# Kernel optimization log

Measured on AMD Instinct MI355X. Metric: run time of the kernel, lower is better.

The kernel has to match this reference:

```python
import jax, jax.numpy as jnp
import numpy as np

B, L, H, E = 4, 2048, 8, 64

def setup_inputs() -> dict:
    key = jax.random.key(0)
    kq, kk, kv = jax.random.split(key, 3)
    queries = jax.random.normal(kq, (B, L, H, E), dtype=jnp.float32)
    keys = jax.random.normal(kk, (B, L, H, E), dtype=jnp.float32)
    values = jax.random.normal(kv, (B, L, H, E), dtype=jnp.float32)
    return {"queries": queries, "keys": keys, "values": values}

def reference(queries, keys, values):
    # queries/keys/values: [B, L, H, E]
    E_ = queries.shape[-1]
    scale = 1.0 / jnp.sqrt(jnp.float32(E_))
    # scores: [B, H, L, S]
    scores = jnp.einsum('blhe,bshe->bhls', queries, keys)
    Lq, S = scores.shape[-2], scores.shape[-1]
    # TriangularCausalMask: mask positions where s > l (strict upper triangle)
    causal = jnp.tril(jnp.ones((Lq, S), dtype=bool))
    scores = jnp.where(causal, scores, -jnp.inf)
    A = jax.nn.softmax(scale * scores, axis=-1)  # dropout p=0 -> identity
    V = jnp.einsum('bhls,bshd->blhd', A, values)
    return V
```

## Files before the change

### kernel.cpp

```cpp
#include <hip/hip_runtime.h>
#include <hip/hip_bf16.h>


#define Bc 4
#define Lc 2048
#define Hc 8
#define Ec 64
#define TB 64
#define NT (Lc / TB)
#define BH_BYTES (NT * TB * Ec * 2)
#define WS_V_OFF ((size_t)32 * BH_BYTES)

using f32x4 = __attribute__((ext_vector_type(4))) float;
using f16x8 = __attribute__((ext_vector_type(8))) _Float16;
using f16x4 = __attribute__((ext_vector_type(4))) _Float16;
using hf16x2 = __fp16 __attribute__((ext_vector_type(2)));

static __device__ __forceinline__ unsigned int pk2(float lo, float hi) {
    union { hf16x2 h; unsigned int u; } c;
    c.h = __builtin_amdgcn_cvt_pkrtz(lo, hi);
    return c.u;
}

static __device__ __forceinline__ void gload16(const void* g, void* l) {
    __builtin_amdgcn_global_load_lds(
        (const __attribute__((address_space(1))) unsigned int*)g,
        (__attribute__((address_space(3))) unsigned int*)l, 16, 0, 0);
}

__global__ __launch_bounds__(256)
void prep_kernel(const float* __restrict__ K, const float* __restrict__ V,
                 char* __restrict__ ws)
{
    __shared__ char vstage[64 * 144];

    const int bid = blockIdx.x;
    const int bh = bid >> 5, kt = bid & 31;
    const int b = bh >> 3, h = bh & 7;
    const int tid = threadIdx.x;
    const int r = tid >> 2, q4 = tid & 3;
    const int c0 = 16 * q4;
    const size_t base_bh = (size_t)b * Lc * Hc * Ec + (size_t)h * Ec;
    const int kbase = kt * TB;
    char* kimg = ws + (size_t)bh * BH_BYTES + (size_t)kt * 8192;
    char* vimg = ws + WS_V_OFF + (size_t)bh * BH_BYTES + (size_t)kt * 8192;

    const int rs = (r & 7) << 4;
    {
        const float* kp = K + base_bh + (size_t)(kbase + r) * 512 + c0;
        unsigned int w[8];
        #pragma unroll
        for (int i = 0; i < 4; ++i) {
            float4 f = *(const float4*)(kp + 4 * i);
            w[2*i]   = pk2(f.x, f.y);
            w[2*i+1] = pk2(f.z, f.w);
        }
        *(uint4*)(kimg + r * 128 + ((32*q4)      ^ rs)) = *(uint4*)&w[0];
        *(uint4*)(kimg + r * 128 + ((32*q4 + 16) ^ rs)) = *(uint4*)&w[4];
    }
    {
        const float* vp = V + base_bh + (size_t)(kbase + r) * 512 + c0;
        unsigned int w[8];
        #pragma unroll
        for (int i = 0; i < 4; ++i) {
            float4 f = *(const float4*)(vp + 4 * i);
            w[2*i]   = pk2(f.x, f.y);
            w[2*i+1] = pk2(f.z, f.w);
        }
        *(uint4*)(vstage + r * 144 + 32*q4)      = *(uint4*)&w[0];
        *(uint4*)(vstage + r * 144 + 32*q4 + 16) = *(uint4*)&w[4];
    }
    __syncthreads();
    {
        const int e = tid >> 2, kq = tid & 3, kv0 = 16 * kq;
        unsigned int w[8];
        #pragma unroll
        for (int i = 0; i < 8; ++i) {
            unsigned int lo = *(const unsigned short*)(vstage + (kv0 + 2*i)     * 144 + 2*e);
            unsigned int hi = *(const unsigned short*)(vstage + (kv0 + 2*i + 1) * 144 + 2*e);
            w[i] = lo | (hi << 16);
        }
        const int es = (e & 7) << 4;
        *(uint4*)(vimg + e * 128 + ((32*kq)      ^ es)) = *(uint4*)&w[0];
        *(uint4*)(vimg + e * 128 + ((32*kq + 16) ^ es)) = *(uint4*)&w[4];
    }
}

__global__ __launch_bounds__(128, 3)
void fa_fwd_kernel(const float* __restrict__ Q, const char* __restrict__ ws,
                   float* __restrict__ Out)
{
    __shared__ char klds[2 * 8192];
    __shared__ char vlds[2 * 8192];

    const int bid = blockIdx.x;
    const int qi  = bid >> 5;
    const int bh  = bid & 31;
    const int b   = bh >> 3, h = bh & 7;
    const int qt  = (NT - 1) - qi;
    const int qbase = qt * TB;

    const int tid  = threadIdx.x;
    const int wid  = tid >> 6;
    const int lane = tid & 63;
    const int l15  = lane & 15;
    const int l4   = lane >> 4;

    const size_t base_bh = (size_t)b * Lc * Hc * Ec + (size_t)h * Ec;
    const char* kimg = ws + (size_t)bh * BH_BYTES;
    const char* vimg = ws + WS_V_OFF + (size_t)bh * BH_BYTES;
    const float SL2E = 0.125f * 1.44269504088896340736f;

    const int sw  = (l15 & 7) << 4;
    const int ko0 = l15 * 128 + ((16 * l4)      ^ sw);
    const int ko1 = l15 * 128 + ((64 + 16 * l4) ^ sw);
    int vo[4];
    #pragma unroll
    for (int m = 0; m < 4; ++m) vo[m] = l15 * 128 + ((32 * m + 8 * l4) ^ sw);

    f16x4 ones;
    {
        const _Float16 ov = (_Float16)((l15 == 0) ? 1.0f : 0.0f);
        ones[0] = ov; ones[1] = ov; ones[2] = ov; ones[3] = ov;
    }

    const int stoff = tid * 16;

    f16x8 qa[2][2];
    #pragma unroll
    for (int g = 0; g < 2; ++g) {
        const int qrow = qbase + 32 * wid + 16 * g + l15;
        const float* qpr = Q + base_bh + (size_t)qrow * 512 + 8 * l4;
        float4 f0 = *(const float4*)(qpr);
        float4 f1 = *(const float4*)(qpr + 4);
        float4 f2 = *(const float4*)(qpr + 32);
        float4 f3 = *(const float4*)(qpr + 36);
        union { f16x8 v; unsigned int u[4]; } pk;
        pk.u[0] = pk2(f0.x * SL2E, f0.y * SL2E);
        pk.u[1] = pk2(f0.z * SL2E, f0.w * SL2E);
        pk.u[2] = pk2(f1.x * SL2E, f1.y * SL2E);
        pk.u[3] = pk2(f1.z * SL2E, f1.w * SL2E);
        qa[g][0] = pk.v;
        pk.u[0] = pk2(f2.x * SL2E, f2.y * SL2E);
        pk.u[1] = pk2(f2.z * SL2E, f2.w * SL2E);
        pk.u[2] = pk2(f3.x * SL2E, f3.y * SL2E);
        pk.u[3] = pk2(f3.z * SL2E, f3.w * SL2E);
        qa[g][1] = pk.v;
    }

    f32x4 o[2][4] = {};
    f32x4 ol[2] = {};
    float m_run[2] = {-1e30f, -1e30f};

    #pragma unroll
    for (int j = 0; j < 4; ++j) {
        gload16(kimg + stoff + j * 2048, klds + stoff + j * 2048);
        gload16(vimg + stoff + j * 2048, vlds + stoff + j * 2048);
    }
    __syncthreads();

    for (int kt = 0; kt <= qt; ++kt) {
        const int cur = kt & 1;
        const char* kb = klds + cur * 8192;
        const char* vb = vlds + cur * 8192;

        if (kt < qt) {
            const char* ks = kimg + (size_t)(kt + 1) * 8192;
            const char* vs = vimg + (size_t)(kt + 1) * 8192;
            char* kd = klds + (cur ^ 1) * 8192;
            char* vd = vlds + (cur ^ 1) * 8192;
            #pragma unroll
            for (int j = 0; j < 4; ++j) {
                gload16(ks + stoff + j * 2048, kd + stoff + j * 2048);
                gload16(vs + stoff + j * 2048, vd + stoff + j * 2048);
            }
        }

        f32x4 s[2][4];
        #pragma unroll
        for (int n = 0; n < 4; ++n) {
            f16x8 a0 = *(const f16x8*)(kb + n * 2048 + ko0);
            f16x8 a1 = *(const f16x8*)(kb + n * 2048 + ko1);
            #pragma unroll
            for (int g = 0; g < 2; ++g) {
                f32x4 z = {0.f, 0.f, 0.f, 0.f};
                z = __builtin_amdgcn_mfma_f32_16x16x32_f16(a0, qa[g][0], z, 0, 0, 0);
                z = __builtin_amdgcn_mfma_f32_16x16x32_f16(a1, qa[g][1], z, 0, 0, 0);
                s[g][n] = z;
            }
        }

        if (kt == qt) {
            #pragma unroll
            for (int g = 0; g < 2; ++g) {
                const int q_g = qbase + 32 * wid + 16 * g + l15;
                #pragma unroll
                for (int n = 0; n < 4; ++n) {
                    #pragma unroll
                    for (int r = 0; r < 4; ++r) {
                        const int kv_g = kt * TB + 16 * n + 4 * l4 + r;
                        if (kv_g > q_g) s[g][n][r] = -1e30f;
                    }
                }
            }
        }

        float pmax[2];
        #pragma unroll
        for (int g = 0; g < 2; ++g) {
            float a0 = fmaxf(s[g][0][0], s[g][0][1]), a1 = fmaxf(s[g][0][2], s[g][0][3]);
            float a2 = fmaxf(s[g][1][0], s[g][1][1]), a3 = fmaxf(s[g][1][2], s[g][1][3]);
            float a4 = fmaxf(s[g][2][0], s[g][2][1]), a5 = fmaxf(s[g][2][2], s[g][2][3]);
            float a6 = fmaxf(s[g][3][0], s[g][3][1]), a7 = fmaxf(s[g][3][2], s[g][3][3]);
            float pm = fmaxf(fmaxf(fmaxf(a0, a1), fmaxf(a2, a3)),
                             fmaxf(fmaxf(a4, a5), fmaxf(a6, a7)));
            pm = fmaxf(pm, __shfl_xor(pm, 16, 64));
            pm = fmaxf(pm, __shfl_xor(pm, 32, 64));
            pmax[g] = pm;
        }

        #pragma unroll
        for (int g = 0; g < 2; ++g) {
            if (!__all(pmax[g] - m_run[g] <= 8.0f)) {
                const float m_new = fmaxf(m_run[g], pmax[g]);
                const float fac = __builtin_exp2f(m_run[g] - m_new);
                m_run[g] = m_new;
                float fr[4];
                #pragma unroll
                for (int r = 0; r < 4; ++r) fr[r] = __shfl(fac, 4 * l4 + r, 64);
                #pragma unroll
                for (int c = 0; c < 4; ++c)
                    #pragma unroll
                    for (int r = 0; r < 4; ++r) o[g][c][r] *= fr[r];
                #pragma unroll
                for (int r = 0; r < 4; ++r) ol[g][r] *= fr[r];
            }
        }

        unsigned int ph[2][4][2];
        #pragma unroll
        for (int g = 0; g < 2; ++g) {
            #pragma unroll
            for (int n = 0; n < 4; ++n) {
                float p0 = __builtin_exp2f(s[g][n][0] - m_run[g]);
                float p1 = __builtin_exp2f(s[g][n][1] - m_run[g]);
                float p2 = __builtin_exp2f(s[g][n][2] - m_run[g]);
                float p3 = __builtin_exp2f(s[g][n][3] - m_run[g]);
                ph[g][n][0] = pk2(p0, p1);
                ph[g][n][1] = pk2(p2, p3);
            }
        }

        #pragma unroll
        for (int m = 0; m < 4; ++m) {
            f16x4 vbf[4];
            #pragma unroll
            for (int c = 0; c < 4; ++c)
                vbf[c] = *(const f16x4*)(vb + c * 2048 + vo[m]);
            #pragma unroll
            for (int g = 0; g < 2; ++g) {
                union { f16x4 h; unsigned int u[2]; } pa;
                pa.u[0] = ph[g][m][0]; pa.u[1] = ph[g][m][1];
                ol[g] = __builtin_amdgcn_mfma_f32_16x16x16f16(pa.h, ones, ol[g], 0, 0, 0);
                #pragma unroll
                for (int c = 0; c < 4; ++c)
                    o[g][c] = __builtin_amdgcn_mfma_f32_16x16x16f16(pa.h, vbf[c], o[g][c], 0, 0, 0);
            }
        }
        __syncthreads();
    }

    float* op = Out + base_bh;
    #pragma unroll
    for (int g = 0; g < 2; ++g) {
        float ir[4];
        #pragma unroll
        for (int r = 0; r < 4; ++r) {
            const float iv = 1.0f / ol[g][r];
            ir[r] = __shfl(iv, 16 * l4, 64);
        }
        const int qrow0 = qbase + 32 * wid + 16 * g;
        #pragma unroll
        for (int c = 0; c < 4; ++c)
            #pragma unroll
            for (int r = 0; r < 4; ++r)
                op[(size_t)(qrow0 + 4 * l4 + r) * 512 + 16 * c + l15] = o[g][c][r] * ir[r];
    }
}

extern "C" void kernel_launch(void* const* d_in, const int* in_sizes, int n_in,
                              void* d_out, int out_size, void* d_ws, size_t ws_size,
                              hipStream_t stream) {
    const float* Q = (const float*)d_in[0];
    const float* K = (const float*)d_in[1];
    const float* V = (const float*)d_in[2];
    float* O = (float*)d_out;
    char* ws = (char*)d_ws;
    hipLaunchKernelGGL(prep_kernel, dim3(Bc * Hc * NT), dim3(256), 0, stream, K, V, ws);
    hipLaunchKernelGGL(fa_fwd_kernel, dim3(NT * Bc * Hc), dim3(128), 0, stream, Q, ws, O);
}
```

Before: 73.30 us.

## Pre-swizzle K/V into MFMA fragment order and load straight to registers

The prep kernel now writes K and V tiles in the exact per-lane MFMA operand layout, so the attention kernel loads them directly from global memory into registers instead of staging them through LDS with barriers. The attention kernel becomes single-wave blocks of 32 query rows (2048 blocks), mapped so each XCD handles a contiguous set of batch-heads for L2 locality, and it prefetches the next K/V tile into registers. This removes LDS traffic and __syncthreads, but raises register pressure and depends on cache bandwidth to keep the per-wave global loads from stalling.

```diff
diff --git a/kernel.cpp b/kernel.cpp
--- a/kernel.cpp
+++ b/kernel.cpp
@@ -1,15 +1,15 @@
 #include <hip/hip_runtime.h>
-#include <hip/hip_bf16.h>
 
 
 #define Bc 4
 #define Lc 2048
 #define Hc 8
 #define Ec 64
-#define TB 64
-#define NT (Lc / TB)
-#define BH_BYTES (NT * TB * Ec * 2)
-#define WS_V_OFF ((size_t)32 * BH_BYTES)
+#define KVT 64
+#define NKV (Lc / KVT)
+#define TILEB 8192
+#define BHB ((size_t)NKV * TILEB)
+#define WSV ((size_t)32 * BHB)
 
 using f32x4 = __attribute__((ext_vector_type(4))) float;
 using f16x8 = __attribute__((ext_vector_type(8))) _Float16;
@@ -22,53 +22,36 @@
     return c.u;
 }
 
-static __device__ __forceinline__ void gload16(const void* g, void* l) {
-    __builtin_amdgcn_global_load_lds(
-        (const __attribute__((address_space(1))) unsigned int*)g,
-        (__attribute__((address_space(3))) unsigned int*)l, 16, 0, 0);
-}
-
 __global__ __launch_bounds__(256)
 void prep_kernel(const float* __restrict__ K, const float* __restrict__ V,
                  char* __restrict__ ws)
 {
-    __shared__ char vstage[64 * 144];
+    __shared__ char kst[64 * 128];
+    __shared__ char vst[64 * 144];
+    __shared__ char vtt[64 * 128];
 
     const int bid = blockIdx.x;
     const int bh = bid >> 5, kt = bid & 31;
     const int b = bh >> 3, h = bh & 7;
     const int tid = threadIdx.x;
-    const int r = tid >> 2, q4 = tid & 3;
-    const int c0 = 16 * q4;
-    const size_t base_bh = (size_t)b * Lc * Hc * Ec + (size_t)h * Ec;
-    const int kbase = kt * TB;
-    char* kimg = ws + (size_t)bh * BH_BYTES + (size_t)kt * 8192;
-    char* vimg = ws + WS_V_OFF + (size_t)bh * BH_BYTES + (size_t)kt * 8192;
-
-    const int rs = (r & 7) << 4;
-    {
-        const float* kp = K + base_bh + (size_t)(kbase + r) * 512 + c0;
-        unsigned int w[8];
+    const size_t base = (size_t)b * Lc * Hc * Ec + (size_t)h * Ec;
+
+    {
+        const int r = tid >> 2, q4 = tid & 3, c0 = 16 * q4;
+        const float* kp = K + base + (size_t)(kt * 64 + r) * 512 + c0;
+        const float* vp = V + base + (size_t)(kt * 64 + r) * 512 + c0;
+        unsigned int wk[8], wv[8];
         #pragma unroll
         for (int i = 0; i < 4; ++i) {
-            float4 f = *(const float4*)(kp + 4 * i);
-            w[2*i]   = pk2(f.x, f.y);
-            w[2*i+1] = pk2(f.z, f.w);
-        }
-        *(uint4*)(kimg + r * 128 + ((32*q4)      ^ rs)) = *(uint4*)&w[0];
-        *(uint4*)(kimg + r * 128 + ((32*q4 + 16) ^ rs)) = *(uint4*)&w[4];
-    }
-    {
-        const float* vp = V + base_bh + (size_t)(kbase + r) * 512 + c0;
-        unsigned int w[8];
-        #pragma unroll
-        for (int i = 0; i < 4; ++i) {
-            float4 f = *(const float4*)(vp + 4 * i);
-            w[2*i]   = pk2(f.x, f.y);
-            w[2*i+1] = pk2(f.z, f.w);
-        }
-        *(uint4*)(vstage + r * 144 + 32*q4)      = *(uint4*)&w[0];
-        *(uint4*)(vstage + r * 144 + 32*q4 + 16) = *(uint4*)&w[4];
+            float4 fk = *(const float4*)(kp + 4 * i);
+            float4 fv = *(const float4*)(vp + 4 * i);
+            wk[2*i]   = pk2(fk.x, fk.y); wk[2*i+1] = pk2(fk.z, fk.w);
+            wv[2*i]   = pk2(fv.x, fv.y); wv[2*i+1] = pk2(fv.z, fv.w);
+        }
+        *(uint4*)(kst + r * 128 + 2 * c0)      = *(uint4*)&wk[0];
+        *(uint4*)(kst + r * 128 + 2 * c0 + 16) = *(uint4*)&wk[4];
+        *(uint4*)(vst + r * 144 + 2 * c0)      = *(uint4*)&wv[0];
+        *(uint4*)(vst + r * 144 + 2 * c0 + 16) = *(uint4*)&wv[4];
     }
     __syncthreads();
     {
@@ -76,47 +59,56 @@
         unsigned int w[8];
         #pragma unroll
         for (int i = 0; i < 8; ++i) {
-            unsigned int lo = *(const unsigned short*)(vstage + (kv0 + 2*i)     * 144 + 2*e);
-            unsigned int hi = *(const unsigned short*)(vstage + (kv0 + 2*i + 1) * 144 + 2*e);
+            unsigned int lo = *(const unsigned short*)(vst + (kv0 + 2*i)     * 144 + 2*e);
+            unsigned int hi = *(const unsigned short*)(vst + (kv0 + 2*i + 1) * 144 + 2*e);
             w[i] = lo | (hi << 16);
         }
-        const int es = (e & 7) << 4;
-        *(uint4*)(vimg + e * 128 + ((32*kq)      ^ es)) = *(uint4*)&w[0];
-        *(uint4*)(vimg + e * 128 + ((32*kq + 16) ^ es)) = *(uint4*)&w[4];
-    }
-}
-
-__global__ __launch_bounds__(128, 3)
+        *(uint4*)(vtt + e * 128 + 2 * kv0)      = *(uint4*)&w[0];
+        *(uint4*)(vtt + e * 128 + 2 * kv0 + 16) = *(uint4*)&w[4];
+    }
+    __syncthreads();
+    {
+        const int lane = tid & 63, qq = tid >> 6;
+        const int l15 = lane & 15, l4 = lane >> 4;
+        char* ko = ws + (size_t)bh * BHB + (size_t)kt * TILEB;
+        char* vo = ws + WSV + (size_t)bh * BHB + (size_t)kt * TILEB;
+        uint4 k0 = *(const uint4*)(kst + (16 * qq + l15) * 128 + 16 * l4);
+        uint4 k1 = *(const uint4*)(kst + (16 * qq + l15) * 128 + 64 + 16 * l4);
+        *(uint4*)(ko + (2 * qq)     * 1024 + lane * 16) = k0;
+        *(uint4*)(ko + (2 * qq + 1) * 1024 + lane * 16) = k1;
+        unsigned long long vv[4];
+        #pragma unroll
+        for (int c = 0; c < 4; ++c)
+            vv[c] = *(const unsigned long long*)(vtt + (16 * c + l15) * 128 + 32 * qq + 8 * l4);
+        uint4 v01, v23;
+        v01.x = (unsigned)vv[0]; v01.y = (unsigned)(vv[0] >> 32);
+        v01.z = (unsigned)vv[1]; v01.w = (unsigned)(vv[1] >> 32);
+        v23.x = (unsigned)vv[2]; v23.y = (unsigned)(vv[2] >> 32);
+        v23.z = (unsigned)vv[3]; v23.w = (unsigned)(vv[3] >> 32);
+        *(uint4*)(vo + (2 * qq)     * 1024 + lane * 16) = v01;
+        *(uint4*)(vo + (2 * qq + 1) * 1024 + lane * 16) = v23;
+    }
+}
+
+__global__ __launch_bounds__(64, 2)
 void fa_fwd_kernel(const float* __restrict__ Q, const char* __restrict__ ws,
                    float* __restrict__ Out)
 {
-    __shared__ char klds[2 * 8192];
-    __shared__ char vlds[2 * 8192];
-
     const int bid = blockIdx.x;
-    const int qi  = bid >> 5;
-    const int bh  = bid & 31;
-    const int b   = bh >> 3, h = bh & 7;
-    const int qt  = (NT - 1) - qi;
-    const int qbase = qt * TB;
-
-    const int tid  = threadIdx.x;
-    const int wid  = tid >> 6;
-    const int lane = tid & 63;
-    const int l15  = lane & 15;
-    const int l4   = lane >> 4;
-
-    const size_t base_bh = (size_t)b * Lc * Hc * Ec + (size_t)h * Ec;
-    const char* kimg = ws + (size_t)bh * BH_BYTES;
-    const char* vimg = ws + WS_V_OFF + (size_t)bh * BH_BYTES;
+    const int xcd = bid & 7;
+    const int rr  = bid >> 3;
+    const int bh  = 4 * xcd + (rr & 3);
+    const int qi  = rr >> 2;
+    const int qt  = 63 - qi;
+    const int steps = (qt >> 1) + 1;
+    const int b = bh >> 3, h = bh & 7;
+
+    const int lane = threadIdx.x;
+    const int l15 = lane & 15, l4 = lane >> 4;
+    const size_t base = (size_t)b * Lc * Hc * Ec + (size_t)h * Ec;
+    const char* kimg = ws + (size_t)bh * BHB + lane * 16;
+    const char* vimg = ws + WSV + (size_t)bh * BHB + lane * 16;
     const float SL2E = 0.125f * 1.44269504088896340736f;
-
-    const int sw  = (l15 & 7) << 4;
-    const int ko0 = l15 * 128 + ((16 * l4)      ^ sw);
-    const int ko1 = l15 * 128 + ((64 + 16 * l4) ^ sw);
-    int vo[4];
-    #pragma unroll
-    for (int m = 0; m < 4; ++m) vo[m] = l15 * 128 + ((32 * m + 8 * l4) ^ sw);
 
     f16x4 ones;
     {
@@ -124,13 +116,11 @@
         ones[0] = ov; ones[1] = ov; ones[2] = ov; ones[3] = ov;
     }
 
-    const int stoff = tid * 16;
-
     f16x8 qa[2][2];
     #pragma unroll
     for (int g = 0; g < 2; ++g) {
-        const int qrow = qbase + 32 * wid + 16 * g + l15;
-        const float* qpr = Q + base_bh + (size_t)qrow * 512 + 8 * l4;
+        const int qrow = qt * 32 + 16 * g + l15;
+        const float* qpr = Q + base + (size_t)qrow * 512 + 8 * l4;
         float4 f0 = *(const float4*)(qpr);
         float4 f1 = *(const float4*)(qpr + 4);
         float4 f2 = *(const float4*)(qpr + 32);
@@ -152,54 +142,44 @@
     f32x4 ol[2] = {};
     float m_run[2] = {-1e30f, -1e30f};
 
-    #pragma unroll
-    for (int j = 0; j < 4; ++j) {
-        gload16(kimg + stoff + j * 2048, klds + stoff + j * 2048);
-        gload16(vimg + stoff + j * 2048, vlds + stoff + j * 2048);
-    }
-    __syncthreads();
-
-    for (int kt = 0; kt <= qt; ++kt) {
-        const int cur = kt & 1;
-        const char* kb = klds + cur * 8192;
-        const char* vb = vlds + cur * 8192;
-
-        if (kt < qt) {
-            const char* ks = kimg + (size_t)(kt + 1) * 8192;
-            const char* vs = vimg + (size_t)(kt + 1) * 8192;
-            char* kd = klds + (cur ^ 1) * 8192;
-            char* vd = vlds + (cur ^ 1) * 8192;
-            #pragma unroll
-            for (int j = 0; j < 4; ++j) {
-                gload16(ks + stoff + j * 2048, kd + stoff + j * 2048);
-                gload16(vs + stoff + j * 2048, vd + stoff + j * 2048);
-            }
-        }
-
+    uint4 kf[8], vf[8];
+    #pragma unroll
+    for (int j = 0; j < 8; ++j) kf[j] = *(const uint4*)(kimg + j * 1024);
+    #pragma unroll
+    for (int j = 0; j < 8; ++j) vf[j] = *(const uint4*)(vimg + j * 1024);
+
+    #pragma unroll 1
+    for (int kt = 0; kt < steps; ++kt) {
         f32x4 s[2][4];
         #pragma unroll
         for (int n = 0; n < 4; ++n) {
-            f16x8 a0 = *(const f16x8*)(kb + n * 2048 + ko0);
-            f16x8 a1 = *(const f16x8*)(kb + n * 2048 + ko1);
+            union { uint4 u; f16x8 h; } a0, a1;
+            a0.u = kf[2 * n]; a1.u = kf[2 * n + 1];
             #pragma unroll
             for (int g = 0; g < 2; ++g) {
                 f32x4 z = {0.f, 0.f, 0.f, 0.f};
-                z = __builtin_amdgcn_mfma_f32_16x16x32_f16(a0, qa[g][0], z, 0, 0, 0);
-                z = __builtin_amdgcn_mfma_f32_16x16x32_f16(a1, qa[g][1], z, 0, 0, 0);
+                z = __builtin_amdgcn_mfma_f32_16x16x32_f16(a0.h, qa[g][0], z, 0, 0, 0);
+                z = __builtin_amdgcn_mfma_f32_16x16x32_f16(a1.h, qa[g][1], z, 0, 0, 0);
                 s[g][n] = z;
             }
         }
 
-        if (kt == qt) {
+        if (kt + 1 < steps) {
+            const char* kp = kimg + (size_t)(kt + 1) * TILEB;
+            #pragma unroll
+            for (int j = 0; j < 8; ++j) kf[j] = *(const uint4*)(kp + j * 1024);
+        }
+
+        if (kt == steps - 1) {
             #pragma unroll
             for (int g = 0; g < 2; ++g) {
-                const int q_g = qbase + 32 * wid + 16 * g + l15;
+                const int q_g = qt * 32 + 16 * g + l15;
                 #pragma unroll
                 for (int n = 0; n < 4; ++n) {
                     #pragma unroll
-                    for (int r = 0; r < 4; ++r) {
-                        const int kv_g = kt * TB + 16 * n + 4 * l4 + r;
-                        if (kv_g > q_g) s[g][n][r] = -1e30f;
+                    for (int r2 = 0; r2 < 4; ++r2) {
+                        const int kv_g = kt * 64 + 16 * n + 4 * l4 + r2;
+                        if (kv_g > q_g) s[g][n][r2] = -1e30f;
                     }
                 }
             }
@@ -218,7 +198,6 @@
             pm = fmaxf(pm, __shfl_xor(pm, 32, 64));
             pmax[g] = pm;
         }
-
         #pragma unroll
         for (int g = 0; g < 2; ++g) {
             if (!__all(pmax[g] - m_run[g] <= 8.0f)) {
@@ -227,13 +206,13 @@
                 m_run[g] = m_new;
                 float fr[4];
                 #pragma unroll
-                for (int r = 0; r < 4; ++r) fr[r] = __shfl(fac, 4 * l4 + r, 64);
+                for (int r2 = 0; r2 < 4; ++r2) fr[r2] = __shfl(fac, 4 * l4 + r2, 64);
                 #pragma unroll
                 for (int c = 0; c < 4; ++c)
                     #pragma unroll
-                    for (int r = 0; r < 4; ++r) o[g][c][r] *= fr[r];
-                #pragma unroll
-                for (int r = 0; r < 4; ++r) ol[g][r] *= fr[r];
+                    for (int r2 = 0; r2 < 4; ++r2) o[g][c][r2] *= fr[r2];
+                #pragma unroll
+                for (int r2 = 0; r2 < 4; ++r2) ol[g][r2] *= fr[r2];
             }
         }
 
@@ -253,38 +232,42 @@
 
         #pragma unroll
         for (int m = 0; m < 4; ++m) {
-            f16x4 vbf[4];
-            #pragma unroll
-            for (int c = 0; c < 4; ++c)
-                vbf[c] = *(const f16x4*)(vb + c * 2048 + vo[m]);
+            union { uint4 u; f16x4 h[2]; } w0, w1;
+            w0.u = vf[2 * m]; w1.u = vf[2 * m + 1];
             #pragma unroll
             for (int g = 0; g < 2; ++g) {
                 union { f16x4 h; unsigned int u[2]; } pa;
                 pa.u[0] = ph[g][m][0]; pa.u[1] = ph[g][m][1];
                 ol[g] = __builtin_amdgcn_mfma_f32_16x16x16f16(pa.h, ones, ol[g], 0, 0, 0);
-                #pragma unroll
-                for (int c = 0; c < 4; ++c)
-                    o[g][c] = __builtin_amdgcn_mfma_f32_16x16x16f16(pa.h, vbf[c], o[g][c], 0, 0, 0);
-            }
-        }
-        __syncthreads();
-    }
-
-    float* op = Out + base_bh;
+                o[g][0] = __builtin_amdgcn_mfma_f32_16x16x16f16(pa.h, w0.h[0], o[g][0], 0, 0, 0);
+                o[g][1] = __builtin_amdgcn_mfma_f32_16x16x16f16(pa.h, w0.h[1], o[g][1], 0, 0, 0);
+                o[g][2] = __builtin_amdgcn_mfma_f32_16x16x16f16(pa.h, w1.h[0], o[g][2], 0, 0, 0);
+                o[g][3] = __builtin_amdgcn_mfma_f32_16x16x16f16(pa.h, w1.h[1], o[g][3], 0, 0, 0);
+            }
+        }
+
+        if (kt + 1 < steps) {
+            const char* vp2 = vimg + (size_t)(kt + 1) * TILEB;
+            #pragma unroll
+            for (int j = 0; j < 8; ++j) vf[j] = *(const uint4*)(vp2 + j * 1024);
+        }
+    }
+
+    float* op = Out + base;
     #pragma unroll
     for (int g = 0; g < 2; ++g) {
         float ir[4];
         #pragma unroll
-        for (int r = 0; r < 4; ++r) {
-            const float iv = 1.0f / ol[g][r];
-            ir[r] = __shfl(iv, 16 * l4, 64);
-        }
-        const int qrow0 = qbase + 32 * wid + 16 * g;
+        for (int r2 = 0; r2 < 4; ++r2) {
+            const float iv = 1.0f / ol[g][r2];
+            ir[r2] = __shfl(iv, 16 * l4, 64);
+        }
+        const int qrow0 = qt * 32 + 16 * g;
         #pragma unroll
         for (int c = 0; c < 4; ++c)
             #pragma unroll
-            for (int r = 0; r < 4; ++r)
-                op[(size_t)(qrow0 + 4 * l4 + r) * 512 + 16 * c + l15] = o[g][c][r] * ir[r];
+            for (int r2 = 0; r2 < 4; ++r2)
+                op[(size_t)(qrow0 + 4 * l4 + r2) * 512 + 16 * c + l15] = o[g][c][r2] * ir[r2];
     }
 }
 
@@ -296,6 +279,6 @@
     const float* V = (const float*)d_in[2];
     float* O = (float*)d_out;
     char* ws = (char*)d_ws;
-    hipLaunchKernelGGL(prep_kernel, dim3(Bc * Hc * NT), dim3(256), 0, stream, K, V, ws);
-    hipLaunchKernelGGL(fa_fwd_kernel, dim3(NT * Bc * Hc), dim3(128), 0, stream, Q, ws, O);
-}
+    hipLaunchKernelGGL(prep_kernel, dim3(32 * NKV), dim3(256), 0, stream, K, V, ws);
+    hipLaunchKernelGGL(fa_fwd_kernel, dim3(2048), dim3(64), 0, stream, Q, ws, O);
+}
```

Result: faster. 60.92 us (-16.9%).
